# Performance work log

Hardware: AMD Instinct MI355X
Metric: run time of the kernel (lower is better)

Reference implementation:

```python
import jax, jax.numpy as jnp
import numpy as np

K = 3  # involution kernel size


def dwconv3x3(x, w, b):
    # x: [B,C,H,W], w: [C,1,3,3] (depthwise, groups=C), b: [C]
    y = jax.lax.conv_general_dilated(
        x, w, window_strides=(1, 1), padding='SAME',
        dimension_numbers=('NCHW', 'OIHW', 'NCHW'),
        feature_group_count=x.shape[1])
    return y + b[None, :, None, None]


def conv1x1(x, w, b):
    # x: [B,C,H,W], w: [O,C], b: [O]
    return jnp.einsum('oc,bchw->bohw', w, x) + b[None, :, None, None]


def extract_patches(x):
    # x: [B,C,H,W] -> [B,C,K*K,H,W], zero-padded 'same' 3x3 neighborhoods
    B, C, H, W = x.shape
    p = (K - 1) // 2
    xp = jnp.pad(x, ((0, 0), (0, 0), (p, p), (p, p)))
    return jnp.stack([xp[:, :, i:i + H, j:j + W]
                      for i in range(K) for j in range(K)], axis=2)


def involution(x, w_red, b_red, w_span, b_span):
    # dynamic per-pixel kernels: [B, K*K, H, W]
    kern = conv1x1(jax.nn.relu(conv1x1(x, w_red, b_red)), w_span, b_span)
    patches = extract_patches(x)                 # [B,C,KK,H,W]
    return jnp.einsum('bkhw,bckhw->bchw', kern, patches)


def setup_inputs() -> dict:
    key = jax.random.key(0)
    ks = jax.random.split(key, 10)
    dim, red = 256, 64  # reduction ratio 4
    B, H, W = 8, 64, 64
    s = 0.05
    return {
        'x': jax.random.normal(ks[0], (B, dim, H, W), jnp.float32),
        'w_in': jax.random.normal(ks[1], (dim, 1, 3, 3), jnp.float32) * s,
        'b_in': jax.random.normal(ks[2], (dim,), jnp.float32) * s,
        'w_red': jax.random.normal(ks[3], (red, dim), jnp.float32) * s,
        'b_red': jax.random.normal(ks[4], (red,), jnp.float32) * s,
        'w_span': jax.random.normal(ks[5], (K * K, red), jnp.float32) * s,
        'b_span': jax.random.normal(ks[6], (K * K,), jnp.float32) * s,
        'w_out': jax.random.normal(ks[7], (dim, 1, 3, 3), jnp.float32) * s,
        'b_out': jax.random.normal(ks[8], (dim,), jnp.float32) * s,
    }


def reference(x, w_in, b_in, w_red, b_red, w_span, b_span, w_out, b_out):
    x = dwconv3x3(x, w_in, b_in)
    x = involution(x, w_red, b_red, w_span, b_span)
    x = dwconv3x3(x, w_out, b_out)
    return x
```

## Files before the change

### kernel.cpp

```cpp
#include <hip/hip_runtime.h>

#define BB 8
#define CC 256
#define HH 64
#define WW 64
#define RED 64
#define HW 4096
#define AST 72
#define LS 68

typedef __attribute__((ext_vector_type(8))) short s8v;
typedef __attribute__((ext_vector_type(4))) float f4v;

__device__ __forceinline__ unsigned short f2bf(float f) {
    unsigned u = __float_as_uint(f);
    u += 0x7fff + ((u >> 16) & 1);
    return (unsigned short)(u >> 16);
}

__global__ __launch_bounds__(256) void build_wtf(const float* __restrict__ w_red,
                                                 unsigned short* __restrict__ wtf) {
    int e = blockIdx.x * 256 + threadIdx.x;
    int j = e & 7, l = (e >> 3) & 63, nt = (e >> 9) & 3, kbg = e >> 11;
    int o = nt * 16 + (l & 15);
    int c = kbg * 32 + ((l >> 4) & 3) * 8 + j;
    wtf[e] = f2bf(w_red[o * CC + c]);
}

__global__ __launch_bounds__(512, 4) void dw_kern(const float* __restrict__ x,
                                                  const float* __restrict__ w_in,
                                                  const float* __restrict__ b_in,
                                                  const unsigned short* __restrict__ wtf,
                                                  const float* __restrict__ b_red,
                                                  const float* __restrict__ w_span,
                                                  const float* __restrict__ b_span,
                                                  float* __restrict__ kern) {
    alignas(16) __shared__ char smem[16640 + 18432];
    unsigned short* xs = (unsigned short*)smem;
    float* r_lds = (float*)smem;
    float* part  = (float*)(smem + 16640);

    const int t  = threadIdx.x;
    const int bx = blockIdx.x;
    const int h  = ((bx & 7) << 3) | (bx >> 3);
    const int b  = blockIdx.y;
    const int l  = t & 63;
    const int wv = t >> 6;
    const int mt = wv & 3, nh = wv >> 2;
    const int m0 = mt << 4;
    const int q  = t & 15;
    const int w0 = q << 2;
    const int cr = t >> 4;

    float4 pv[2][3]; float plf[2][3], prt[2][3];

    auto loadX = [&](int c0) {
        #pragma unroll
        for (int s = 0; s < 2; s++) {
            const int cc = c0 + s * 32 + cr;
            const float* xp = x + ((size_t)(b * CC + cc)) * HW;
            #pragma unroll
            for (int ky = 0; ky < 3; ky++) {
                int hh = h + ky - 1;
                if (hh < 0 || hh >= HH) {
                    pv[s][ky] = make_float4(0.f, 0.f, 0.f, 0.f);
                    plf[s][ky] = 0.f; prt[s][ky] = 0.f;
                    continue;
                }
                const float* row = xp + hh * WW + w0;
                pv[s][ky]  = *(const float4*)row;
                plf[s][ky] = (w0 > 0)      ? row[-1] : 0.f;
                prt[s][ky] = (w0 + 4 < WW) ? row[4]  : 0.f;
            }
        }
    };
    auto computeA = [&](int c0) {
        #pragma unroll
        for (int s = 0; s < 2; s++) {
            const int cl = s * 32 + cr;
            const int cc = c0 + cl;
            const float* wp = w_in + cc * 9;
            const float bb = b_in[cc];
            float4 a4 = make_float4(bb, bb, bb, bb);
            #pragma unroll
            for (int ky = 0; ky < 3; ky++) {
                float4 v = pv[s][ky];
                float lf = plf[s][ky], rt = prt[s][ky];
                float k0 = wp[ky * 3 + 0], k1 = wp[ky * 3 + 1], k2 = wp[ky * 3 + 2];
                a4.x = fmaf(k0, lf,  a4.x); a4.y = fmaf(k0, v.x, a4.y);
                a4.z = fmaf(k0, v.y, a4.z); a4.w = fmaf(k0, v.z, a4.w);
                a4.x = fmaf(k1, v.x, a4.x); a4.y = fmaf(k1, v.y, a4.y);
                a4.z = fmaf(k1, v.z, a4.z); a4.w = fmaf(k1, v.w, a4.w);
                a4.x = fmaf(k2, v.y, a4.x); a4.y = fmaf(k2, v.z, a4.y);
                a4.z = fmaf(k2, v.w, a4.z); a4.w = fmaf(k2, rt,  a4.w);
            }
            xs[(w0 + 0) * AST + cl] = f2bf(a4.x);
            xs[(w0 + 1) * AST + cl] = f2bf(a4.y);
            xs[(w0 + 2) * AST + cl] = f2bf(a4.z);
            xs[(w0 + 3) * AST + cl] = f2bf(a4.w);
        }
    };

    s8v bfr[2][2];
    auto loadB = [&](int k) {
        #pragma unroll
        for (int kb = 0; kb < 2; kb++)
            #pragma unroll
            for (int ntl = 0; ntl < 2; ntl++) {
                int nt = (nh << 1) + ntl;
                int kbg = (k << 1) + kb;
                bfr[kb][ntl] = *(const s8v*)(wtf + (((kbg * 4 + nt) * 64 + l) << 3));
            }
    };

    f4v acc[2] = {{0.f, 0.f, 0.f, 0.f}, {0.f, 0.f, 0.f, 0.f}};

    loadX(0); loadB(0);
    for (int k = 0; k < 4; k++) {
        computeA(k << 6);
        if (k < 3) loadX((k + 1) << 6);
        __syncthreads();
        #pragma unroll
        for (int kb = 0; kb < 2; kb++) {
            const unsigned short* ap =
                xs + (m0 + (l & 15)) * AST + (kb << 5) + ((l >> 4) & 3) * 8;
            s8v av = *(const s8v*)ap;
            #pragma unroll
            for (int ntl = 0; ntl < 2; ntl++)
                acc[ntl] = __builtin_amdgcn_mfma_f32_16x16x32_bf16(
                    av, bfr[kb][ntl], acc[ntl], 0, 0, 0);
        }
        if (k < 3) loadB(k + 1);
        __syncthreads();
    }

    #pragma unroll
    for (int ntl = 0; ntl < 2; ntl++) {
        int o = ((nh << 1) + ntl) * 16 + (l & 15);
        int pxr = m0 + ((l >> 4) & 3) * 4;
        #pragma unroll
        for (int i = 0; i < 4; i++)
            r_lds[o * 65 + pxr + i] = acc[ntl][i];
    }
    __syncthreads();

    const int px = t & 63;
    const int o0 = __builtin_amdgcn_readfirstlane(wv << 3);
    float kk[9];
    #pragma unroll
    for (int j = 0; j < 9; j++) kk[j] = 0.f;
    #pragma unroll
    for (int i = 0; i < 8; i++) {
        float r = fmaxf(r_lds[(o0 + i) * 65 + px] + b_red[o0 + i], 0.f);
        #pragma unroll
        for (int j = 0; j < 9; j++) kk[j] = fmaf(w_span[j * RED + o0 + i], r, kk[j]);
    }
    #pragma unroll
    for (int j = 0; j < 9; j++) part[(wv * 9 + j) * 64 + px] = kk[j];
    __syncthreads();
    if (wv == 0) {
        float* kp = kern + (size_t)b * 9 * HW + h * WW + px;
        #pragma unroll
        for (int j = 0; j < 9; j++) {
            float s = b_span[j];
            #pragma unroll
            for (int g = 0; g < 8; g++) s += part[(g * 9 + j) * 64 + px];
            kp[j * HW] = s;
        }
    }
}

__global__ __launch_bounds__(256) void invol_dw(const float* __restrict__ x,
                                                const float* __restrict__ w_in,
                                                const float* __restrict__ b_in,
                                                const float* __restrict__ kern,
                                                const float* __restrict__ w_out,
                                                const float* __restrict__ b_out,
                                                float* __restrict__ out) {
    __shared__ float xs[HH * LS];
    __shared__ float x1s[HH * LS];
    const int t  = threadIdx.x;
    const int q  = t & 15;
    const int w0 = q << 2;
    const int r  = t >> 4;
    const int c = blockIdx.x, b = blockIdx.y;
    const float* xp = x + ((size_t)(b * CC + c)) * HW;

    #pragma unroll
    for (int i = 0; i < 4; i++) {
        int h = r + (i << 4);
        *(float4*)&xs[h * LS + w0] = *(const float4*)(xp + h * WW + w0);
    }
    __syncthreads();

    {
        const float* wp = w_in + c * 9;
        const float bb = b_in[c];
        #pragma unroll
        for (int i = 0; i < 4; i++) {
            int h = r + (i << 4);
            float4 acc = make_float4(bb, bb, bb, bb);
            #pragma unroll
            for (int ky = 0; ky < 3; ky++) {
                int hh = h + ky - 1;
                if (hh < 0 || hh >= HH) continue;
                const float* row = &xs[hh * LS + w0];
                float4 v = *(const float4*)row;
                float lf = (w0 > 0)      ? row[-1] : 0.f;
                float rt = (w0 + 4 < WW) ? row[4]  : 0.f;
                float k0 = wp[ky * 3 + 0], k1 = wp[ky * 3 + 1], k2 = wp[ky * 3 + 2];
                acc.x = fmaf(k0, lf,  acc.x); acc.y = fmaf(k0, v.x, acc.y);
                acc.z = fmaf(k0, v.y, acc.z); acc.w = fmaf(k0, v.z, acc.w);
                acc.x = fmaf(k1, v.x, acc.x); acc.y = fmaf(k1, v.y, acc.y);
                acc.z = fmaf(k1, v.z, acc.z); acc.w = fmaf(k1, v.w, acc.w);
                acc.x = fmaf(k2, v.y, acc.x); acc.y = fmaf(k2, v.z, acc.y);
                acc.z = fmaf(k2, v.w, acc.z); acc.w = fmaf(k2, rt,  acc.w);
            }
            *(float4*)&x1s[h * LS + w0] = acc;
        }
    }
    __syncthreads();

    const float* kp = kern + (size_t)b * 9 * HW;
    #pragma unroll
    for (int i = 0; i < 4; i++) {
        int h  = r + (i << 4);
        int hw = h * WW + w0;
        float4 acc = make_float4(0.f, 0.f, 0.f, 0.f);
        #pragma unroll
        for (int ky = 0; ky < 3; ky++) {
            int hh = h + ky - 1;
            if (hh < 0 || hh >= HH) continue;
            const float* row = &x1s[hh * LS + w0];
            float4 v = *(const float4*)row;
            float lf = (w0 > 0)      ? row[-1] : 0.f;
            float rt = (w0 + 4 < WW) ? row[4]  : 0.f;
            float4 k0 = *(const float4*)(kp + (ky * 3 + 0) * HW + hw);
            float4 k1 = *(const float4*)(kp + (ky * 3 + 1) * HW + hw);
            float4 k2 = *(const float4*)(kp + (ky * 3 + 2) * HW + hw);
            acc.x = fmaf(k0.x, lf,  acc.x); acc.y = fmaf(k0.y, v.x, acc.y);
            acc.z = fmaf(k0.z, v.y, acc.z); acc.w = fmaf(k0.w, v.z, acc.w);
            acc.x = fmaf(k1.x, v.x, acc.x); acc.y = fmaf(k1.y, v.y, acc.y);
            acc.z = fmaf(k1.z, v.z, acc.z); acc.w = fmaf(k1.w, v.w, acc.w);
            acc.x = fmaf(k2.x, v.y, acc.x); acc.y = fmaf(k2.y, v.z, acc.y);
            acc.z = fmaf(k2.z, v.w, acc.z); acc.w = fmaf(k2.w, rt,  acc.w);
        }
        *(float4*)&xs[h * LS + w0] = acc;
    }
    __syncthreads();

    const float* wp = w_out + c * 9;
    const float bb = b_out[c];
    float* op = out + ((size_t)(b * CC + c)) * HW;
    #pragma unroll
    for (int i = 0; i < 4; i++) {
        int h = r + (i << 4);
        float4 acc = make_float4(bb, bb, bb, bb);
        #pragma unroll
        for (int ky = 0; ky < 3; ky++) {
            int hh = h + ky - 1;
            if (hh < 0 || hh >= HH) continue;
            const float* row = &xs[hh * LS + w0];
            float4 v = *(const float4*)row;
            float lf = (w0 > 0)      ? row[-1] : 0.f;
            float rt = (w0 + 4 < WW) ? row[4]  : 0.f;
            float k0 = wp[ky * 3 + 0], k1 = wp[ky * 3 + 1], k2 = wp[ky * 3 + 2];
            acc.x = fmaf(k0, lf,  acc.x); acc.y = fmaf(k0, v.x, acc.y);
            acc.z = fmaf(k0, v.y, acc.z); acc.w = fmaf(k0, v.z, acc.w);
            acc.x = fmaf(k1, v.x, acc.x); acc.y = fmaf(k1, v.y, acc.y);
            acc.z = fmaf(k1, v.z, acc.z); acc.w = fmaf(k1, v.w, acc.w);
            acc.x = fmaf(k2, v.y, acc.x); acc.y = fmaf(k2, v.z, acc.y);
            acc.z = fmaf(k2, v.w, acc.z); acc.w = fmaf(k2, rt,  acc.w);
        }
        *(float4*)(op + h * WW + w0) = acc;
    }
}

extern "C" void kernel_launch(void* const* d_in, const int* in_sizes, int n_in,
                              void* d_out, int out_size, void* d_ws, size_t ws_size,
                              hipStream_t stream) {
    const float* x      = (const float*)d_in[0];
    const float* w_in   = (const float*)d_in[1];
    const float* b_in   = (const float*)d_in[2];
    const float* w_red  = (const float*)d_in[3];
    const float* b_red  = (const float*)d_in[4];
    const float* w_span = (const float*)d_in[5];
    const float* b_span = (const float*)d_in[6];
    const float* w_out  = (const float*)d_in[7];
    const float* b_out  = (const float*)d_in[8];
    float* out = (float*)d_out;

    float* ws   = (float*)d_ws;
    float* kern = ws;
    unsigned short* wtf = (unsigned short*)(kern + (size_t)BB * 9 * HW);

    build_wtf<<<64, 256, 0, stream>>>(w_red, wtf);
    dw_kern<<<dim3(HH, BB), 512, 0, stream>>>(x, w_in, b_in, wtf, b_red,
                                              w_span, b_span, kern);
    invol_dw<<<dim3(CC, BB), 256, 0, stream>>>(x, w_in, b_in, kern,
                                               w_out, b_out, out);
}
```

Before: 136.4 us.

## Drop weight-prep kernel and reuse dynamic kernels across channel groups in register

Removes the separate bf16 weight-packing kernel; dw_kern now loads fp32 w_red directly and converts it to bf16 fragments inline. invol_dw now uses 1024-thread blocks, one thread per 4 pixels. Each block processes a group of 4 channels and keeps the 9 per-pixel involution kernels in registers. This cuts kernel-map global reads by 4x and saves one launch. In exchange there are more syncthreads per channel, register pressure from 36 held floats, and 4x fewer blocks (512).

```diff
diff --git a/kernel.cpp b/kernel.cpp
--- a/kernel.cpp
+++ b/kernel.cpp
@@ -8,6 +8,7 @@
 #define HW 4096
 #define AST 72
 #define LS 68
+#define G  4
 
 typedef __attribute__((ext_vector_type(8))) short s8v;
 typedef __attribute__((ext_vector_type(4))) float f4v;
@@ -18,19 +19,10 @@
     return (unsigned short)(u >> 16);
 }
 
-__global__ __launch_bounds__(256) void build_wtf(const float* __restrict__ w_red,
-                                                 unsigned short* __restrict__ wtf) {
-    int e = blockIdx.x * 256 + threadIdx.x;
-    int j = e & 7, l = (e >> 3) & 63, nt = (e >> 9) & 3, kbg = e >> 11;
-    int o = nt * 16 + (l & 15);
-    int c = kbg * 32 + ((l >> 4) & 3) * 8 + j;
-    wtf[e] = f2bf(w_red[o * CC + c]);
-}
-
 __global__ __launch_bounds__(512, 4) void dw_kern(const float* __restrict__ x,
                                                   const float* __restrict__ w_in,
                                                   const float* __restrict__ b_in,
-                                                  const unsigned short* __restrict__ wtf,
+                                                  const float* __restrict__ w_red,
                                                   const float* __restrict__ b_red,
                                                   const float* __restrict__ w_span,
                                                   const float* __restrict__ b_span,
@@ -107,9 +99,17 @@
         for (int kb = 0; kb < 2; kb++)
             #pragma unroll
             for (int ntl = 0; ntl < 2; ntl++) {
-                int nt = (nh << 1) + ntl;
-                int kbg = (k << 1) + kb;
-                bfr[kb][ntl] = *(const s8v*)(wtf + (((kbg * 4 + nt) * 64 + l) << 3));
+                int o = ((nh << 1) + ntl) * 16 + (l & 15);
+                int c = (k << 6) + (kb << 5) + ((l >> 4) & 3) * 8;
+                const float* wp = w_red + o * CC + c;
+                float4 a  = *(const float4*)wp;
+                float4 b4 = *(const float4*)(wp + 4);
+                s8v f;
+                f[0] = (short)f2bf(a.x);  f[1] = (short)f2bf(a.y);
+                f[2] = (short)f2bf(a.z);  f[3] = (short)f2bf(a.w);
+                f[4] = (short)f2bf(b4.x); f[5] = (short)f2bf(b4.y);
+                f[6] = (short)f2bf(b4.z); f[7] = (short)f2bf(b4.w);
+                bfr[kb][ntl] = f;
             }
     };
 
@@ -170,39 +170,43 @@
     }
 }
 
-__global__ __launch_bounds__(256) void invol_dw(const float* __restrict__ x,
-                                                const float* __restrict__ w_in,
-                                                const float* __restrict__ b_in,
-                                                const float* __restrict__ kern,
-                                                const float* __restrict__ w_out,
-                                                const float* __restrict__ b_out,
-                                                float* __restrict__ out) {
+__global__ __launch_bounds__(1024, 4) void invol_dw(const float* __restrict__ x,
+                                                    const float* __restrict__ w_in,
+                                                    const float* __restrict__ b_in,
+                                                    const float* __restrict__ kern,
+                                                    const float* __restrict__ w_out,
+                                                    const float* __restrict__ b_out,
+                                                    float* __restrict__ out) {
     __shared__ float xs[HH * LS];
     __shared__ float x1s[HH * LS];
     const int t  = threadIdx.x;
-    const int q  = t & 15;
-    const int w0 = q << 2;
     const int r  = t >> 4;
-    const int c = blockIdx.x, b = blockIdx.y;
-    const float* xp = x + ((size_t)(b * CC + c)) * HW;
-
-    #pragma unroll
-    for (int i = 0; i < 4; i++) {
-        int h = r + (i << 4);
-        *(float4*)&xs[h * LS + w0] = *(const float4*)(xp + h * WW + w0);
-    }
-    __syncthreads();
-
+    const int w0 = (t & 15) << 2;
+    const int cg = blockIdx.x;
+    const int b  = blockIdx.y;
+    const int hw = r * WW + w0;
+
+    float4 kv[9];
     {
-        const float* wp = w_in + c * 9;
-        const float bb = b_in[c];
-        #pragma unroll
-        for (int i = 0; i < 4; i++) {
-            int h = r + (i << 4);
+        const float* kp = kern + (size_t)b * 9 * HW + hw;
+        #pragma unroll
+        for (int j = 0; j < 9; j++) kv[j] = *(const float4*)(kp + j * HW);
+    }
+
+    for (int g = 0; g < G; g++) {
+        const int c = cg * G + g;
+        const float* xp = x + ((size_t)(b * CC + c)) * HW;
+
+        *(float4*)&xs[r * LS + w0] = *(const float4*)(xp + hw);
+        __syncthreads();
+
+        {
+            const float* wp = w_in + c * 9;
+            const float bb = b_in[c];
             float4 acc = make_float4(bb, bb, bb, bb);
             #pragma unroll
             for (int ky = 0; ky < 3; ky++) {
-                int hh = h + ky - 1;
+                int hh = r + ky - 1;
                 if (hh < 0 || hh >= HH) continue;
                 const float* row = &xs[hh * LS + w0];
                 float4 v = *(const float4*)row;
@@ -216,63 +220,56 @@
                 acc.x = fmaf(k2, v.y, acc.x); acc.y = fmaf(k2, v.z, acc.y);
                 acc.z = fmaf(k2, v.w, acc.z); acc.w = fmaf(k2, rt,  acc.w);
             }
-            *(float4*)&x1s[h * LS + w0] = acc;
-        }
-    }
-    __syncthreads();
-
-    const float* kp = kern + (size_t)b * 9 * HW;
-    #pragma unroll
-    for (int i = 0; i < 4; i++) {
-        int h  = r + (i << 4);
-        int hw = h * WW + w0;
-        float4 acc = make_float4(0.f, 0.f, 0.f, 0.f);
-        #pragma unroll
-        for (int ky = 0; ky < 3; ky++) {
-            int hh = h + ky - 1;
-            if (hh < 0 || hh >= HH) continue;
-            const float* row = &x1s[hh * LS + w0];
-            float4 v = *(const float4*)row;
-            float lf = (w0 > 0)      ? row[-1] : 0.f;
-            float rt = (w0 + 4 < WW) ? row[4]  : 0.f;
-            float4 k0 = *(const float4*)(kp + (ky * 3 + 0) * HW + hw);
-            float4 k1 = *(const float4*)(kp + (ky * 3 + 1) * HW + hw);
-            float4 k2 = *(const float4*)(kp + (ky * 3 + 2) * HW + hw);
-            acc.x = fmaf(k0.x, lf,  acc.x); acc.y = fmaf(k0.y, v.x, acc.y);
-            acc.z = fmaf(k0.z, v.y, acc.z); acc.w = fmaf(k0.w, v.z, acc.w);
-            acc.x = fmaf(k1.x, v.x, acc.x); acc.y = fmaf(k1.y, v.y, acc.y);
-            acc.z = fmaf(k1.z, v.z, acc.z); acc.w = fmaf(k1.w, v.w, acc.w);
-            acc.x = fmaf(k2.x, v.y, acc.x); acc.y = fmaf(k2.y, v.z, acc.y);
-            acc.z = fmaf(k2.z, v.w, acc.z); acc.w = fmaf(k2.w, rt,  acc.w);
-        }
-        *(float4*)&xs[h * LS + w0] = acc;
-    }
-    __syncthreads();
-
-    const float* wp = w_out + c * 9;
-    const float bb = b_out[c];
-    float* op = out + ((size_t)(b * CC + c)) * HW;
-    #pragma unroll
-    for (int i = 0; i < 4; i++) {
-        int h = r + (i << 4);
-        float4 acc = make_float4(bb, bb, bb, bb);
-        #pragma unroll
-        for (int ky = 0; ky < 3; ky++) {
-            int hh = h + ky - 1;
-            if (hh < 0 || hh >= HH) continue;
-            const float* row = &xs[hh * LS + w0];
-            float4 v = *(const float4*)row;
-            float lf = (w0 > 0)      ? row[-1] : 0.f;
-            float rt = (w0 + 4 < WW) ? row[4]  : 0.f;
-            float k0 = wp[ky * 3 + 0], k1 = wp[ky * 3 + 1], k2 = wp[ky * 3 + 2];
-            acc.x = fmaf(k0, lf,  acc.x); acc.y = fmaf(k0, v.x, acc.y);
-            acc.z = fmaf(k0, v.y, acc.z); acc.w = fmaf(k0, v.z, acc.w);
-            acc.x = fmaf(k1, v.x, acc.x); acc.y = fmaf(k1, v.y, acc.y);
-            acc.z = fmaf(k1, v.z, acc.z); acc.w = fmaf(k1, v.w, acc.w);
-            acc.x = fmaf(k2, v.y, acc.x); acc.y = fmaf(k2, v.z, acc.y);
-            acc.z = fmaf(k2, v.w, acc.z); acc.w = fmaf(k2, rt,  acc.w);
-        }
-        *(float4*)(op + h * WW + w0) = acc;
+            *(float4*)&x1s[r * LS + w0] = acc;
+        }
+        __syncthreads();
+
+        {
+            float4 acc = make_float4(0.f, 0.f, 0.f, 0.f);
+            #pragma unroll
+            for (int ky = 0; ky < 3; ky++) {
+                int hh = r + ky - 1;
+                if (hh < 0 || hh >= HH) continue;
+                const float* row = &x1s[hh * LS + w0];
+                float4 v = *(const float4*)row;
+                float lf = (w0 > 0)      ? row[-1] : 0.f;
+                float rt = (w0 + 4 < WW) ? row[4]  : 0.f;
+                float4 k0 = kv[ky * 3 + 0], k1 = kv[ky * 3 + 1], k2 = kv[ky * 3 + 2];
+                acc.x = fmaf(k0.x, lf,  acc.x); acc.y = fmaf(k0.y, v.x, acc.y);
+                acc.z = fmaf(k0.z, v.y, acc.z); acc.w = fmaf(k0.w, v.z, acc.w);
+                acc.x = fmaf(k1.x, v.x, acc.x); acc.y = fmaf(k1.y, v.y, acc.y);
+                acc.z = fmaf(k1.z, v.z, acc.z); acc.w = fmaf(k1.w, v.w, acc.w);
+                acc.x = fmaf(k2.x, v.y, acc.x); acc.y = fmaf(k2.y, v.z, acc.y);
+                acc.z = fmaf(k2.z, v.w, acc.z); acc.w = fmaf(k2.w, rt,  acc.w);
+            }
+            __syncthreads();
+            *(float4*)&xs[r * LS + w0] = acc;
+        }
+        __syncthreads();
+
+        {
+            const float* wp = w_out + c * 9;
+            const float bb = b_out[c];
+            float4 acc = make_float4(bb, bb, bb, bb);
+            #pragma unroll
+            for (int ky = 0; ky < 3; ky++) {
+                int hh = r + ky - 1;
+                if (hh < 0 || hh >= HH) continue;
+                const float* row = &xs[hh * LS + w0];
+                float4 v = *(const float4*)row;
+                float lf = (w0 > 0)      ? row[-1] : 0.f;
+                float rt = (w0 + 4 < WW) ? row[4]  : 0.f;
+                float k0 = wp[ky * 3 + 0], k1 = wp[ky * 3 + 1], k2 = wp[ky * 3 + 2];
+                acc.x = fmaf(k0, lf,  acc.x); acc.y = fmaf(k0, v.x, acc.y);
+                acc.z = fmaf(k0, v.y, acc.z); acc.w = fmaf(k0, v.z, acc.w);
+                acc.x = fmaf(k1, v.x, acc.x); acc.y = fmaf(k1, v.y, acc.y);
+                acc.z = fmaf(k1, v.z, acc.z); acc.w = fmaf(k1, v.w, acc.w);
+                acc.x = fmaf(k2, v.y, acc.x); acc.y = fmaf(k2, v.z, acc.y);
+                acc.z = fmaf(k2, v.w, acc.z); acc.w = fmaf(k2, rt,  acc.w);
+            }
+            *(float4*)(out + ((size_t)(b * CC + c)) * HW + hw) = acc;
+        }
+        __syncthreads();
     }
 }
 
@@ -290,13 +287,10 @@
     const float* b_out  = (const float*)d_in[8];
     float* out = (float*)d_out;
 
-    float* ws   = (float*)d_ws;
-    float* kern = ws;
-    unsigned short* wtf = (unsigned short*)(kern + (size_t)BB * 9 * HW);
-
-    build_wtf<<<64, 256, 0, stream>>>(w_red, wtf);
-    dw_kern<<<dim3(HH, BB), 512, 0, stream>>>(x, w_in, b_in, wtf, b_red,
+    float* kern = (float*)d_ws;
+
+    dw_kern<<<dim3(HH, BB), 512, 0, stream>>>(x, w_in, b_in, w_red, b_red,
                                               w_span, b_span, kern);
-    invol_dw<<<dim3(CC, BB), 256, 0, stream>>>(x, w_in, b_in, kern,
-                                               w_out, b_out, out);
-}
+    invol_dw<<<dim3(CC / G, BB), 1024, 0, stream>>>(x, w_in, b_in, kern,
+                                                    w_out, b_out, out);
+}
```

Result: slower. 156.0 us (+14.3%).
